# Kernel optimization log

Hardware: AMD Instinct MI355X
Metric: run time of the kernel (lower is better)

Reference implementation:

```python
import jax, jax.numpy as jnp
import numpy as np

MAP_SHAPE = (40, 50)   # SOM grid -> L = 2000 landmarks
NUM_FEATURE = 64
BATCH = 2048
R = 1.0
GAMMA = 1.0 / (2.0 * R ** 2)


def _make_qd():
    # Pairwise squared distances between 2D grid coordinates, Gaussian kernel.
    ii, jj = np.meshgrid(np.arange(MAP_SHAPE[0]), np.arange(MAP_SHAPE[1]), indexing='ij')
    coords = np.stack([ii.ravel(), jj.ravel()], axis=1).astype(np.float32)  # (L, 2)
    d2 = ((coords[:, None, :] - coords[None, :, :]) ** 2).sum(-1)           # (L, L)
    return jnp.asarray(np.exp(-GAMMA * d2), dtype=jnp.float32)


def setup_inputs() -> dict:
    key = jax.random.key(0)
    kx, kl = jax.random.split(key)
    x = jax.random.normal(kx, (BATCH, NUM_FEATURE), dtype=jnp.float32)
    landmarks = jax.random.normal(kl, (MAP_SHAPE[0] * MAP_SHAPE[1], NUM_FEATURE), dtype=jnp.float32)
    qd = _make_qd()
    return {"x": x, "landmarks": landmarks, "qd": qd}


def reference(x, landmarks, qd):
    # Squared Euclidean distances: (B, L)
    xlm = x @ landmarks.T
    x2 = jnp.sum(jnp.square(x), axis=1, keepdims=True)        # (B, 1)
    lm2 = jnp.sum(jnp.square(landmarks), axis=1)               # (L,)
    d = x2 + lm2 - 2.0 * xlm                                   # (B, L)
    min_idx = jnp.argmin(d, axis=-1)                            # (B,) BMU index
    h = qd[min_idx]                                             # (B, L) neighborhood weights
    # delta0[b, l, f] = h[b, l] * (x[b, f] - landmarks[l, f])
    delta0 = h[:, :, None] * (x[:, None, :] - landmarks[None, :, :])  # (B, L, F)
    return delta0
```

## Files before the change

### kernel.cpp

```cpp
#include <hip/hip_runtime.h>

#define L_LM 2000
#define F_DIM 64
#define B_SZ 2048

typedef float f32x4 __attribute__((ext_vector_type(4)));

__global__ __launch_bounds__(256) void som_bmu_kernel(
    const float* __restrict__ x, const float* __restrict__ lm,
    int* __restrict__ min_idx)
{
    constexpr int ROWS = 8;
    const int b0 = blockIdx.x * ROWS;
    const int tid = threadIdx.x;

    __shared__ float xs[ROWS][F_DIM];
    for (int i = tid; i < ROWS * F_DIM; i += 256) {
        xs[i / F_DIM][i % F_DIM] = x[(size_t)(b0 + i / F_DIM) * F_DIM + (i % F_DIM)];
    }
    __syncthreads();

    float best[ROWS];
    int   bidx[ROWS];
#pragma unroll
    for (int r = 0; r < ROWS; ++r) { best[r] = 3.4e38f; bidx[r] = 0; }

    for (int l = tid; l < L_LM; l += 256) {
        const float4* lp = reinterpret_cast<const float4*>(lm + (size_t)l * F_DIM);
        float dot[ROWS];
        float l2 = 0.f;
#pragma unroll
        for (int r = 0; r < ROWS; ++r) dot[r] = 0.f;
#pragma unroll
        for (int k = 0; k < F_DIM / 4; ++k) {
            float4 v = lp[k];
            l2 += v.x * v.x + v.y * v.y + v.z * v.z + v.w * v.w;
#pragma unroll
            for (int r = 0; r < ROWS; ++r) {
                dot[r] += v.x * xs[r][4 * k + 0] + v.y * xs[r][4 * k + 1]
                        + v.z * xs[r][4 * k + 2] + v.w * xs[r][4 * k + 3];
            }
        }
#pragma unroll
        for (int r = 0; r < ROWS; ++r) {
            float s = l2 - 2.f * dot[r];
            if (s < best[r]) { best[r] = s; bidx[r] = l; }
        }
    }

#pragma unroll
    for (int r = 0; r < ROWS; ++r) {
        float s = best[r]; int i = bidx[r];
        for (int off = 32; off > 0; off >>= 1) {
            float s2 = __shfl_down(s, off);
            int   i2 = __shfl_down(i, off);
            if (s2 < s || (s2 == s && i2 < i)) { s = s2; i = i2; }
        }
        best[r] = s; bidx[r] = i;
    }

    __shared__ float sbest[4][ROWS];
    __shared__ int   sidx[4][ROWS];
    const int wave = tid >> 6;
    const int lane = tid & 63;
    if (lane == 0) {
#pragma unroll
        for (int r = 0; r < ROWS; ++r) { sbest[wave][r] = best[r]; sidx[wave][r] = bidx[r]; }
    }
    __syncthreads();
    if (tid < ROWS) {
        float s = sbest[0][tid]; int i = sidx[0][tid];
#pragma unroll
        for (int w = 1; w < 4; ++w) {
            float s2 = sbest[w][tid]; int i2 = sidx[w][tid];
            if (s2 < s || (s2 == s && i2 < i)) { s = s2; i = i2; }
        }
        min_idx[b0 + tid] = i;
    }
}

__global__ __launch_bounds__(256) void som_h_kernel(
    const float* __restrict__ qd, const int* __restrict__ min_idx,
    f32x4* __restrict__ hs4)
{
    constexpr unsigned NH4 = (unsigned)B_SZ * (L_LM / 4);
    constexpr unsigned RH4 = L_LM / 4;
    const f32x4* __restrict__ qd4 = reinterpret_cast<const f32x4*>(qd);
    const unsigned stride = gridDim.x * 256u;
    for (unsigned i = blockIdx.x * 256u + threadIdx.x; i < NH4; i += stride) {
        const unsigned b = i / RH4;
        const unsigned c = i - b * RH4;
        const unsigned bmu = (unsigned)min_idx[b];
        hs4[i] = qd4[bmu * RH4 + c];
    }
}

__global__ __launch_bounds__(256) void som_delta_kernel(
    const float* __restrict__ x, const float* __restrict__ lm,
    const float* __restrict__ hs, f32x4* __restrict__ out)
{
    constexpr unsigned N4   = (unsigned)B_SZ * L_LM * (F_DIM / 4);
    constexpr unsigned ROW4 = L_LM * (F_DIM / 4);
    const unsigned stride = gridDim.x * 256u;
    const f32x4* __restrict__ lmv = reinterpret_cast<const f32x4*>(lm);
    const f32x4* __restrict__ xv4 = reinterpret_cast<const f32x4*>(x);

#pragma unroll 5
    for (unsigned g4 = blockIdx.x * 256u + threadIdx.x; g4 < N4; g4 += stride) {
        const unsigned b   = g4 / ROW4;
        const unsigned rem = g4 - b * ROW4;
        const float h  = hs[(size_t)(g4 >> 4)];
        const f32x4 lv = lmv[rem];
        const f32x4 xv = xv4[(b << 4) | (rem & 15u)];
        f32x4 o;
        o.x = h * (xv.x - lv.x);
        o.y = h * (xv.y - lv.y);
        o.z = h * (xv.z - lv.z);
        o.w = h * (xv.w - lv.w);
        __builtin_nontemporal_store(o, &out[g4]);
    }
}

extern "C" void kernel_launch(void* const* d_in, const int* in_sizes, int n_in,
                              void* d_out, int out_size, void* d_ws, size_t ws_size,
                              hipStream_t stream) {
    const float* x  = (const float*)d_in[0];
    const float* lm = (const float*)d_in[1];
    const float* qd = (const float*)d_in[2];
    float* out = (float*)d_out;

    int*   midx = (int*)d_ws;
    float* hs   = (float*)((char*)d_ws + (1u << 20));

    som_bmu_kernel<<<B_SZ / 8, 256, 0, stream>>>(x, lm, midx);
    som_h_kernel<<<1024, 256, 0, stream>>>(qd, midx, (f32x4*)hs);
    som_delta_kernel<<<2048, 256, 0, stream>>>(x, lm, hs, (f32x4*)out);
}
```

Before: 289.4 us.

## Tile delta kernel into 80-landmark spans staged through shared memory

The delta kernel now gives each block a sequence of 80-landmark spans of one batch row. Each span's landmark slice and h values are staged in LDS, then written out as contiguous nontemporal stores. The per-element integer division by the row size goes away, along with redundant h loads. The cost is two barriers per span and a strict dependence on the 2048x25 span count matching the grid and step count.

```diff
diff --git a/kernel.cpp b/kernel.cpp
--- a/kernel.cpp
+++ b/kernel.cpp
@@ -3,6 +3,11 @@
 #define L_LM 2000
 #define F_DIM 64
 #define B_SZ 2048
+#define SPAN_L 80
+#define SPANS_PER_ROW 25
+#define SPAN_F4 (SPAN_L * F_DIM / 4)
+#define DELTA_GRID 2048
+#define KSTEPS 25
 
 typedef float f32x4 __attribute__((ext_vector_type(4)));
 
@@ -90,8 +95,7 @@
     for (unsigned i = blockIdx.x * 256u + threadIdx.x; i < NH4; i += stride) {
         const unsigned b = i / RH4;
         const unsigned c = i - b * RH4;
-        const unsigned bmu = (unsigned)min_idx[b];
-        hs4[i] = qd4[bmu * RH4 + c];
+        hs4[i] = qd4[(unsigned)min_idx[b] * RH4 + c];
     }
 }
 
@@ -99,25 +103,39 @@
     const float* __restrict__ x, const float* __restrict__ lm,
     const float* __restrict__ hs, f32x4* __restrict__ out)
 {
-    constexpr unsigned N4   = (unsigned)B_SZ * L_LM * (F_DIM / 4);
-    constexpr unsigned ROW4 = L_LM * (F_DIM / 4);
-    const unsigned stride = gridDim.x * 256u;
-    const f32x4* __restrict__ lmv = reinterpret_cast<const f32x4*>(lm);
-    const f32x4* __restrict__ xv4 = reinterpret_cast<const f32x4*>(x);
+    __shared__ float lms[SPAN_L * F_DIM];
+    __shared__ float hls[SPAN_L];
+    const int t = threadIdx.x;
+    f32x4* lms4 = reinterpret_cast<f32x4*>(lms);
+    const f32x4* __restrict__ lm4 = reinterpret_cast<const f32x4*>(lm);
+    const f32x4* __restrict__ x4  = reinterpret_cast<const f32x4*>(x);
 
-#pragma unroll 5
-    for (unsigned g4 = blockIdx.x * 256u + threadIdx.x; g4 < N4; g4 += stride) {
-        const unsigned b   = g4 / ROW4;
-        const unsigned rem = g4 - b * ROW4;
-        const float h  = hs[(size_t)(g4 >> 4)];
-        const f32x4 lv = lmv[rem];
-        const f32x4 xv = xv4[(b << 4) | (rem & 15u)];
-        f32x4 o;
-        o.x = h * (xv.x - lv.x);
-        o.y = h * (xv.y - lv.y);
-        o.z = h * (xv.z - lv.z);
-        o.w = h * (xv.w - lv.w);
-        __builtin_nontemporal_store(o, &out[g4]);
+    for (int k = 0; k < KSTEPS; ++k) {
+        const unsigned s  = (unsigned)k * DELTA_GRID + blockIdx.x;
+        const unsigned b  = s / SPANS_PER_ROW;
+        const unsigned sr = s - b * SPANS_PER_ROW;
+
+#pragma unroll
+        for (int j = 0; j < 5; ++j)
+            lms4[j * 256 + t] = lm4[sr * SPAN_F4 + j * 256 + t];
+        if (t < SPAN_L) hls[t] = hs[b * (unsigned)L_LM + sr * SPAN_L + t];
+        const f32x4 xv = x4[(b << 4) | (t & 15u)];
+        __syncthreads();
+
+        f32x4* __restrict__ ob = out + (size_t)s * SPAN_F4;
+#pragma unroll
+        for (int j = 0; j < 5; ++j) {
+            const int idx = j * 256 + t;
+            const float h  = hls[idx >> 4];
+            const f32x4 lv = lms4[idx];
+            f32x4 o;
+            o.x = h * (xv.x - lv.x);
+            o.y = h * (xv.y - lv.y);
+            o.z = h * (xv.z - lv.z);
+            o.w = h * (xv.w - lv.w);
+            __builtin_nontemporal_store(o, &ob[idx]);
+        }
+        __syncthreads();
     }
 }
 
@@ -134,5 +152,5 @@
 
     som_bmu_kernel<<<B_SZ / 8, 256, 0, stream>>>(x, lm, midx);
     som_h_kernel<<<1024, 256, 0, stream>>>(qd, midx, (f32x4*)hs);
-    som_delta_kernel<<<2048, 256, 0, stream>>>(x, lm, hs, (f32x4*)out);
+    som_delta_kernel<<<DELTA_GRID, 256, 0, stream>>>(x, lm, hs, (f32x4*)out);
 }
```

After: 275.4 us. -4.9%, faster.

## Restructure delta kernel into per-wave spans with register double-buffered prefetch

Applied to the files above, without the earlier changes.

The delta kernel now gives each wave a 16-landmark span of one batch row and walks spans with a fixed stride. It double-buffers landmark, h and x loads in registers so the next span's loads are in flight while the current span's four nontemporal stores are issued. This replaces the generic grid-stride loop and its per-element division with one division per span, aiming to hide load latency behind the write-bound output stream. Grid size changes to 2000 blocks and the loop count is hardcoded to cover exactly B*L/16 spans, so the code only works for these fixed shapes.

```diff
diff --git a/kernel.cpp b/kernel.cpp
--- a/kernel.cpp
+++ b/kernel.cpp
@@ -3,6 +3,13 @@
 #define L_LM 2000
 #define F_DIM 64
 #define B_SZ 2048
+
+#define SPAN_L 16
+#define SPANS_PER_ROW 125
+#define SPAN_F4 256
+#define DGRID 2000
+#define WAVES_TOT (DGRID * 4)
+#define DK 32
 
 typedef float f32x4 __attribute__((ext_vector_type(4)));
 
@@ -90,8 +97,7 @@
     for (unsigned i = blockIdx.x * 256u + threadIdx.x; i < NH4; i += stride) {
         const unsigned b = i / RH4;
         const unsigned c = i - b * RH4;
-        const unsigned bmu = (unsigned)min_idx[b];
-        hs4[i] = qd4[bmu * RH4 + c];
+        hs4[i] = qd4[(unsigned)min_idx[b] * RH4 + c];
     }
 }
 
@@ -99,26 +105,60 @@
     const float* __restrict__ x, const float* __restrict__ lm,
     const float* __restrict__ hs, f32x4* __restrict__ out)
 {
-    constexpr unsigned N4   = (unsigned)B_SZ * L_LM * (F_DIM / 4);
-    constexpr unsigned ROW4 = L_LM * (F_DIM / 4);
-    const unsigned stride = gridDim.x * 256u;
-    const f32x4* __restrict__ lmv = reinterpret_cast<const f32x4*>(lm);
-    const f32x4* __restrict__ xv4 = reinterpret_cast<const f32x4*>(x);
+    const int lane = threadIdx.x & 63;
+    const int gw   = (blockIdx.x << 2) | (threadIdx.x >> 6);
+    const unsigned s4 = (unsigned)(lane >> 4);
+    const unsigned f4 = (unsigned)(lane & 15);
+    const f32x4* __restrict__ lm4 = reinterpret_cast<const f32x4*>(lm);
+    const f32x4* __restrict__ x4  = reinterpret_cast<const f32x4*>(x);
 
-#pragma unroll 5
-    for (unsigned g4 = blockIdx.x * 256u + threadIdx.x; g4 < N4; g4 += stride) {
-        const unsigned b   = g4 / ROW4;
-        const unsigned rem = g4 - b * ROW4;
-        const float h  = hs[(size_t)(g4 >> 4)];
-        const f32x4 lv = lmv[rem];
-        const f32x4 xv = xv4[(b << 4) | (rem & 15u)];
-        f32x4 o;
-        o.x = h * (xv.x - lv.x);
-        o.y = h * (xv.y - lv.y);
-        o.z = h * (xv.z - lv.z);
-        o.w = h * (xv.w - lv.w);
-        __builtin_nontemporal_store(o, &out[g4]);
+#define PREFETCH(SP, L0, L1, L2, L3, H0, H1, H2, H3, XV)                  \
+    {                                                                     \
+        const unsigned bb_ = (SP) / (unsigned)SPANS_PER_ROW;              \
+        const unsigned sr_ = (SP) - bb_ * (unsigned)SPANS_PER_ROW;        \
+        const f32x4* lp_ = lm4 + sr_ * (unsigned)SPAN_F4;                 \
+        L0 = lp_[lane];        L1 = lp_[64 + lane];                       \
+        L2 = lp_[128 + lane];  L3 = lp_[192 + lane];                      \
+        const float* hp_ = hs + bb_ * (unsigned)L_LM + sr_ * 16u + s4;    \
+        H0 = hp_[0]; H1 = hp_[4]; H2 = hp_[8]; H3 = hp_[12];              \
+        XV = x4[(bb_ << 4) | f4];                                         \
     }
+
+#define STORESPAN(SP, L0, L1, L2, L3, H0, H1, H2, H3, XV)                 \
+    {                                                                     \
+        f32x4* ob_ = out + (size_t)(SP) * SPAN_F4 + lane;                 \
+        f32x4 o_;                                                         \
+        o_.x = H0 * (XV.x - L0.x); o_.y = H0 * (XV.y - L0.y);             \
+        o_.z = H0 * (XV.z - L0.z); o_.w = H0 * (XV.w - L0.w);             \
+        __builtin_nontemporal_store(o_, &ob_[0]);                         \
+        o_.x = H1 * (XV.x - L1.x); o_.y = H1 * (XV.y - L1.y);             \
+        o_.z = H1 * (XV.z - L1.z); o_.w = H1 * (XV.w - L1.w);             \
+        __builtin_nontemporal_store(o_, &ob_[64]);                        \
+        o_.x = H2 * (XV.x - L2.x); o_.y = H2 * (XV.y - L2.y);             \
+        o_.z = H2 * (XV.z - L2.z); o_.w = H2 * (XV.w - L2.w);             \
+        __builtin_nontemporal_store(o_, &ob_[128]);                       \
+        o_.x = H3 * (XV.x - L3.x); o_.y = H3 * (XV.y - L3.y);             \
+        o_.z = H3 * (XV.z - L3.z); o_.w = H3 * (XV.w - L3.w);             \
+        __builtin_nontemporal_store(o_, &ob_[192]);                       \
+    }
+
+    f32x4 a0, a1, a2, a3, xa;  float ha0, ha1, ha2, ha3;
+    f32x4 c0, c1, c2, c3, xc;  float hc0, hc1, hc2, hc3;
+
+    unsigned span = (unsigned)gw;
+    PREFETCH(span, a0, a1, a2, a3, ha0, ha1, ha2, ha3, xa);
+
+    for (int k = 0; k < DK; k += 2) {
+        const unsigned sp1 = span + WAVES_TOT;
+        const unsigned sp2 = (k + 2 < DK) ? sp1 + WAVES_TOT : sp1;
+        PREFETCH(sp1, c0, c1, c2, c3, hc0, hc1, hc2, hc3, xc);
+        STORESPAN(span, a0, a1, a2, a3, ha0, ha1, ha2, ha3, xa);
+        PREFETCH(sp2, a0, a1, a2, a3, ha0, ha1, ha2, ha3, xa);
+        STORESPAN(sp1, c0, c1, c2, c3, hc0, hc1, hc2, hc3, xc);
+        span = sp2;
+    }
+#undef PREFETCH
+#undef STORESPAN
 }
 
 extern "C" void kernel_launch(void* const* d_in, const int* in_sizes, int n_in,
@@ -134,5 +174,5 @@
 
     som_bmu_kernel<<<B_SZ / 8, 256, 0, stream>>>(x, lm, midx);
     som_h_kernel<<<1024, 256, 0, stream>>>(qd, midx, (f32x4*)hs);
-    som_delta_kernel<<<2048, 256, 0, stream>>>(x, lm, hs, (f32x4*)out);
+    som_delta_kernel<<<DGRID, 256, 0, stream>>>(x, lm, hs, (f32x4*)out);
 }
```

New measurement: 277.4 us. 4.2% less time.
